# Kernel tuning notes

Measured on AMD Instinct MI355X. Metric: run time of the kernel, lower is better.

## Reference

```python
import jax, jax.numpy as jnp
import numpy as np


def floor_ste(x):
    # forward: floor(x); backward: identity (straight-through estimator)
    return x + jax.lax.stop_gradient(jnp.floor(x) - x)


def _int_polynomial(x_int, sf):
    c0, c1, c2 = 0.35815147, 0.96963238, 1.0
    b_int = floor_ste((c1 / c0) / sf)
    c_int = floor_ste((c2 / c0) / (sf * sf))
    z = x_int * (x_int + b_int) + c_int
    return z, c0 * sf * sf


def _int_exp(x_int, sf):
    x0 = -0.69314718
    n = 15
    x0_int = floor_ste(x0 / sf)
    x_int = jnp.maximum(x_int, n * x0_int)
    q = floor_ste(x_int / x0_int)
    r = x_int - x0_int * q
    exp_int, exp_sf = _int_polynomial(r, sf)
    exp_int = jnp.maximum(floor_ste(exp_int * jnp.exp2(n - q)), 0.0)
    return exp_int, exp_sf / (2.0 ** n)


def _int_softmax(x, sf):
    x_int = x / sf
    x_int = x_int - jnp.max(x_int, axis=-1, keepdims=True)
    exp_int, exp_sf = _int_exp(x_int, sf)
    exp_int_sum = jnp.sum(exp_int, axis=-1, keepdims=True)
    return exp_int, exp_int_sum, exp_sf


def setup_inputs() -> dict:
    key = jax.random.key(0)
    k1, = jax.random.split(key, 1)
    x = jax.random.normal(k1, (2, 16, 1024, 1024), dtype=jnp.float32)
    scale = jnp.float32(0.05)          # activation quantization step
    threshold = jnp.array([0.1], dtype=jnp.float32)  # nn.Parameter init
    return {"x": x, "scale": scale, "threshold": threshold}


def reference(x, scale, threshold):
    output_bit = 8
    threshold_bits = 8
    exp_int, exp_int_sum, exp_sf = _int_softmax(x, scale)
    factor = floor_ste((2.0 ** 32) / exp_int_sum)
    out_scale_A = threshold / (2.0 ** output_bit - 1.0)   # shape [1]
    out_scale_B = 1.0 / (2.0 ** output_bit - 1.0)
    approx_threshold = (floor_ste(threshold * 2.0 ** threshold_bits)
                        * exp_int_sum / (2.0 ** threshold_bits))
    mask_A = exp_int <= approx_threshold
    exp_int_A = jnp.where(mask_A, exp_int, 0.0)
    exp_int_B = jnp.where(mask_A, 0.0, exp_int)
    softmax_int_A = floor_ste(exp_int_A * factor / ((2.0 ** 32) * out_scale_A))
    softmax_int_B = floor_ste(exp_int_B * factor / ((2.0 ** 32) * out_scale_B))
    softmax_int_B = jnp.minimum(softmax_int_B, 255.0)
    return softmax_int_A * out_scale_A + softmax_int_B * out_scale_B
```

## Files before the change

kernel.cpp:

```cpp
#include <hip/hip_runtime.h>
#include <math.h>

#pragma clang fp contract(off)

#define TPB 256
#define ROWLEN 1024

typedef float f32x4 __attribute__((ext_vector_type(4)));

__global__ __launch_bounds__(TPB) void qsplit_int_softmax_kernel(
    const float* __restrict__ x,
    const float* __restrict__ scale_p,
    const float* __restrict__ thr_p,
    float* __restrict__ out)
{
    const int lane = threadIdx.x & 63;
    const int wid  = threadIdx.x >> 6;
    const int row  = blockIdx.x * 4 + wid;
    const size_t rbase = (size_t)row * ROWLEN + (size_t)lane * 4;

    const float sf  = scale_p[0];
    const float thr = thr_p[0];

    const double sfd  = (double)sf;
    const double rd   = 1.0 / sfd;
    const float  rh   = (float)rd;
    const float  rl   = (float)(rd - (double)rh);

    const double x0d    = floor(-0.69314718 / sfd);
    const float  x0f    = (float)x0d;
    const float  bfc    = (float)floor((0.96963238 / 0.35815147) / sfd);
    const float  cfc    = (float)floor((1.0 / 0.35815147) / (sfd * sfd));
    const float  clampf = (float)(15.0 * x0d);
    const float  invx0f = (float)(1.0 / x0d);

    f32x4 xv[4];
    #pragma unroll
    for (int k = 0; k < 4; ++k)
        xv[k] = *(const f32x4*)(x + rbase + (size_t)k * 256);

    float xi[16];
    #pragma unroll
    for (int k = 0; k < 4; ++k) {
        #pragma unroll
        for (int jj = 0; jj < 4; ++jj) {
            const float xx = xv[k][jj];
            const float p  = xx * rh;
            const float e  = __builtin_fmaf(xx, rh, -p);
            xi[k*4+jj]     = p + __builtin_fmaf(xx, rl, e);
        }
    }

    float m = xi[0];
    #pragma unroll
    for (int j = 1; j < 16; ++j) m = fmaxf(m, xi[j]);
    #pragma unroll
    for (int off = 1; off < 64; off <<= 1)
        m = fmaxf(m, __shfl_xor(m, off));

    float e16[16];
    unsigned int usum = 0;
    #pragma unroll
    for (int j = 0; j < 16; ++j) {
        float v = xi[j] - m;
        v = fmaxf(v, clampf);
        const float qf = floorf(v * invx0f);
        const int   qi = (int)qf;
        const float r  = v - x0f * qf;
        const float t  = r + bfc;
        const float z  = r * t + cfc;
        float ei = floorf(ldexpf(z, 15 - qi));
        ei = fmaxf(ei, 0.0f);
        e16[j] = ei;
        usum += (unsigned int)ei;
    }

    unsigned long long ws = usum;
    #pragma unroll
    for (int off = 1; off < 64; off <<= 1)
        ws += __shfl_xor(ws, off);
    const double s = (double)ws;

    const double factor_d = floor(4294967296.0 / s);
    const float  fac_f = (float)factor_d;
    const float  ath_f = (float)((floor((double)thr * 256.0) * s) * (1.0 / 256.0));

    const float  osA  = thr / 255.0f;
    const float  osB  = 1.0f / 255.0f;
    const float  invA = (float)(1.0 / (4294967296.0 * (double)osA));
    const float  invB = (float)(1.0 / (4294967296.0 * (double)osB));

    #pragma unroll
    for (int k = 0; k < 4; ++k) {
        f32x4 o;
        #pragma unroll
        for (int jj = 0; jj < 4; ++jj) {
            const float ei  = e16[k*4+jj];
            const bool  isA = (ei <= ath_f);
            const float t1  = ei * fac_f;
            const float t2  = t1 * (isA ? invA : invB);
            float si = floorf(t2);
            si = fminf(si, isA ? 3.0e38f : 255.0f);
            o[jj] = si * (isA ? osA : osB);
        }
        __builtin_nontemporal_store(o, (f32x4*)(out + rbase + (size_t)k * 256));
    }
}

extern "C" void kernel_launch(void* const* d_in, const int* in_sizes, int n_in,
                              void* d_out, int out_size, void* d_ws, size_t ws_size,
                              hipStream_t stream) {
    const float* x     = (const float*)d_in[0];
    const float* scale = (const float*)d_in[1];
    const float* thr   = (const float*)d_in[2];
    float* out = (float*)d_out;

    const int total = in_sizes[0];
    const int rows  = total / ROWLEN;
    const int blocks = rows / 4;

    qsplit_int_softmax_kernel<<<dim3(blocks), dim3(TPB), 0, stream>>>(
        x, scale, thr, out);
}
```

Measured before the change: 232.0 us.

## Process four rows per wave with software-prefetched next-row loads

Each wave now handles four consecutive rows instead of one, loading the next row's data into registers while computing the current row. The grid shrinks by four, amortizing the per-wave scalar setup (double-precision constants from scale and threshold) and hiding global load latency within a wave. The risk is higher register pressure and fewer resident waves, which could reduce the memory-level parallelism the hardware gets from occupancy.

```diff
diff --git a/kernel.cpp b/kernel.cpp
--- a/kernel.cpp
+++ b/kernel.cpp
@@ -5,6 +5,7 @@
 
 #define TPB 256
 #define ROWLEN 1024
+#define ROWS_PER_WAVE 4
 
 typedef float f32x4 __attribute__((ext_vector_type(4)));
 
@@ -16,8 +17,9 @@
 {
     const int lane = threadIdx.x & 63;
     const int wid  = threadIdx.x >> 6;
-    const int row  = blockIdx.x * 4 + wid;
-    const size_t rbase = (size_t)row * ROWLEN + (size_t)lane * 4;
+    const int wave_gid = blockIdx.x * 4 + wid;
+    const size_t row0 = (size_t)wave_gid * ROWS_PER_WAVE;
+    const size_t base0 = row0 * ROWLEN + (size_t)lane * 4;
 
     const float sf  = scale_p[0];
     const float thr = thr_p[0];
@@ -34,76 +36,93 @@
     const float  clampf = (float)(15.0 * x0d);
     const float  invx0f = (float)(1.0 / x0d);
 
-    f32x4 xv[4];
-    #pragma unroll
-    for (int k = 0; k < 4; ++k)
-        xv[k] = *(const f32x4*)(x + rbase + (size_t)k * 256);
-
-    float xi[16];
-    #pragma unroll
-    for (int k = 0; k < 4; ++k) {
-        #pragma unroll
-        for (int jj = 0; jj < 4; ++jj) {
-            const float xx = xv[k][jj];
-            const float p  = xx * rh;
-            const float e  = __builtin_fmaf(xx, rh, -p);
-            xi[k*4+jj]     = p + __builtin_fmaf(xx, rl, e);
-        }
-    }
-
-    float m = xi[0];
-    #pragma unroll
-    for (int j = 1; j < 16; ++j) m = fmaxf(m, xi[j]);
-    #pragma unroll
-    for (int off = 1; off < 64; off <<= 1)
-        m = fmaxf(m, __shfl_xor(m, off));
-
-    float e16[16];
-    unsigned int usum = 0;
-    #pragma unroll
-    for (int j = 0; j < 16; ++j) {
-        float v = xi[j] - m;
-        v = fmaxf(v, clampf);
-        const float qf = floorf(v * invx0f);
-        const int   qi = (int)qf;
-        const float r  = v - x0f * qf;
-        const float t  = r + bfc;
-        const float z  = r * t + cfc;
-        float ei = floorf(ldexpf(z, 15 - qi));
-        ei = fmaxf(ei, 0.0f);
-        e16[j] = ei;
-        usum += (unsigned int)ei;
-    }
-
-    unsigned long long ws = usum;
-    #pragma unroll
-    for (int off = 1; off < 64; off <<= 1)
-        ws += __shfl_xor(ws, off);
-    const double s = (double)ws;
-
-    const double factor_d = floor(4294967296.0 / s);
-    const float  fac_f = (float)factor_d;
-    const float  ath_f = (float)((floor((double)thr * 256.0) * s) * (1.0 / 256.0));
-
     const float  osA  = thr / 255.0f;
     const float  osB  = 1.0f / 255.0f;
     const float  invA = (float)(1.0 / (4294967296.0 * (double)osA));
     const float  invB = (float)(1.0 / (4294967296.0 * (double)osB));
+    const double thrq = floor((double)thr * 256.0);
+
+    f32x4 cur[4], nxt[4];
+    #pragma unroll
+    for (int k = 0; k < 4; ++k)
+        cur[k] = *(const f32x4*)(x + base0 + (size_t)k * 256);
 
     #pragma unroll
-    for (int k = 0; k < 4; ++k) {
-        f32x4 o;
+    for (int r = 0; r < ROWS_PER_WAVE; ++r) {
+        const size_t rbase = base0 + (size_t)r * ROWLEN;
+
+        if (r + 1 < ROWS_PER_WAVE) {
+            #pragma unroll
+            for (int k = 0; k < 4; ++k)
+                nxt[k] = *(const f32x4*)(x + rbase + ROWLEN + (size_t)k * 256);
+        }
+
+        float xi[16];
         #pragma unroll
-        for (int jj = 0; jj < 4; ++jj) {
-            const float ei  = e16[k*4+jj];
-            const bool  isA = (ei <= ath_f);
-            const float t1  = ei * fac_f;
-            const float t2  = t1 * (isA ? invA : invB);
-            float si = floorf(t2);
-            si = fminf(si, isA ? 3.0e38f : 255.0f);
-            o[jj] = si * (isA ? osA : osB);
+        for (int k = 0; k < 4; ++k) {
+            #pragma unroll
+            for (int jj = 0; jj < 4; ++jj) {
+                const float xx = cur[k][jj];
+                const float p  = xx * rh;
+                const float e  = __builtin_fmaf(xx, rh, -p);
+                xi[k*4+jj]     = p + __builtin_fmaf(xx, rl, e);
+            }
         }
-        __builtin_nontemporal_store(o, (f32x4*)(out + rbase + (size_t)k * 256));
+
+        float m = xi[0];
+        #pragma unroll
+        for (int j = 1; j < 16; ++j) m = fmaxf(m, xi[j]);
+        #pragma unroll
+        for (int off = 1; off < 64; off <<= 1)
+            m = fmaxf(m, __shfl_xor(m, off));
+
+        float e16[16];
+        unsigned int usum = 0;
+        #pragma unroll
+        for (int j = 0; j < 16; ++j) {
+            float v = xi[j] - m;
+            v = fmaxf(v, clampf);
+            const float qf = floorf(v * invx0f);
+            const int   qi = (int)qf;
+            const float r2 = v - x0f * qf;
+            const float t  = r2 + bfc;
+            const float z  = r2 * t + cfc;
+            float ei = floorf(ldexpf(z, 15 - qi));
+            ei = fmaxf(ei, 0.0f);
+            e16[j] = ei;
+            usum += (unsigned int)ei;
+        }
+
+        unsigned long long wsum = usum;
+        #pragma unroll
+        for (int off = 1; off < 64; off <<= 1)
+            wsum += __shfl_xor(wsum, off);
+        const double s = (double)wsum;
+
+        const double factor_d = floor(4294967296.0 / s);
+        const float  fac_f = (float)factor_d;
+        const float  ath_f = (float)((thrq * s) * (1.0 / 256.0));
+
+        #pragma unroll
+        for (int k = 0; k < 4; ++k) {
+            f32x4 o;
+            #pragma unroll
+            for (int jj = 0; jj < 4; ++jj) {
+                const float ei  = e16[k*4+jj];
+                const bool  isA = (ei <= ath_f);
+                const float t1  = ei * fac_f;
+                const float t2  = t1 * (isA ? invA : invB);
+                float si = floorf(t2);
+                si = fminf(si, isA ? 3.0e38f : 255.0f);
+                o[jj] = si * (isA ? osA : osB);
+            }
+            __builtin_nontemporal_store(o, (f32x4*)(out + rbase + (size_t)k * 256));
+        }
+
+        if (r + 1 < ROWS_PER_WAVE) {
+            #pragma unroll
+            for (int k = 0; k < 4; ++k) cur[k] = nxt[k];
+        }
     }
 }
 
@@ -117,7 +136,8 @@
 
     const int total = in_sizes[0];
     const int rows  = total / ROWLEN;
-    const int blocks = rows / 4;
+    const int waves = rows / ROWS_PER_WAVE;
+    const int blocks = waves / 4;
 
     qsplit_int_softmax_kernel<<<dim3(blocks), dim3(TPB), 0, stream>>>(
         x, scale, thr, out);
```

Measured after the change: 238.9 us. 3.0% more time.
